# Kernel tuning notes

Measured on AMD Instinct MI355X. Metric: run time of the kernel, lower is better.

## Reference

```python
import jax, jax.numpy as jnp
import numpy as np

D_MODEL = 128
N_HEADS = 8
D_K = D_MODEL // N_HEADS
N_TGT = 40000
N_SRC = 40000
N_EDGES = 640000


def setup_inputs() -> dict:
    key = jax.random.key(0)
    ks = jax.random.split(key, 12)
    s = 1.0 / np.sqrt(D_MODEL)
    return {
        "X_tgt": jax.random.normal(ks[0], (N_TGT, D_MODEL), jnp.float32),
        "X_src": jax.random.normal(ks[1], (N_SRC, D_MODEL), jnp.float32),
        "inc_tgt": jax.random.randint(ks[2], (N_EDGES,), 0, N_TGT),
        "inc_src": jax.random.randint(ks[3], (N_EDGES,), 0, N_SRC),
        "num_tgt": N_TGT,
        # weights stored (in, out): y = x @ W
        "Wq": jax.random.normal(ks[4], (D_MODEL, D_MODEL), jnp.float32) * s,
        "Wkv": jax.random.normal(ks[5], (D_MODEL, 2 * D_MODEL), jnp.float32) * s,
        "Wbt": jax.random.normal(ks[6], (D_MODEL, N_HEADS), jnp.float32) * s,
        "Wbs": jax.random.normal(ks[7], (D_MODEL, N_HEADS), jnp.float32) * s,
        "Wgt_w": jax.random.normal(ks[8], (D_MODEL, D_MODEL), jnp.float32) * s,
        "Wgt_b": jnp.zeros((D_MODEL,), jnp.float32),
        "Wgs_w": jax.random.normal(ks[9], (D_MODEL, D_MODEL), jnp.float32) * s,
        "Wgs_b": jnp.zeros((D_MODEL,), jnp.float32),
        "Wo": jax.random.normal(ks[10], (D_MODEL, D_MODEL), jnp.float32) * s,
    }


def reference(X_tgt, X_src, inc_tgt, inc_src, num_tgt, Wq, Wkv, Wbt, Wbs,
              Wgt_w, Wgt_b, Wgs_w, Wgs_b, Wo):
    H, dk = N_HEADS, D_K
    scale = 1.0 / np.sqrt(dk)
    n_src = X_src.shape[0]

    Q = (X_tgt @ Wq).reshape(-1, H, dk)                 # [Nt,H,dk]
    kv = (X_src @ Wkv).reshape(n_src, 2, H, dk)
    K, V = kv[:, 0], kv[:, 1]                           # [Ns,H,dk]

    # per-edge attention scores [E,H]
    scores = (jnp.sum(Q[inc_tgt] * K[inc_src], axis=-1) * scale
              + (X_tgt @ Wbt)[inc_tgt]
              + (X_src @ Wbs)[inc_src])

    # segment softmax over edges grouped by target node
    mx = jax.ops.segment_max(scores, inc_tgt, num_segments=num_tgt)  # [Nt,H]
    exp_s = jnp.exp(scores - mx[inc_tgt])
    sm = jax.ops.segment_sum(exp_s, inc_tgt, num_segments=num_tgt)
    attn = exp_s / (sm[inc_tgt] + 1e-12)                # [E,H]

    g_src = jax.nn.sigmoid(X_src @ Wgs_w + Wgs_b).reshape(n_src, H, dk)
    msg = attn[..., None] * (g_src[inc_src] * V[inc_src])          # [E,H,dk]
    out = jax.ops.segment_sum(msg, inc_tgt, num_segments=num_tgt)  # [Nt,H,dk]

    g_tgt = jax.nn.sigmoid(X_tgt @ Wgt_w + Wgt_b).reshape(-1, H, dk)
    return (g_tgt * out).reshape(-1, H * dk) @ Wo
```

## Files before the change

### kernel.cpp

```cpp
#include <hip/hip_runtime.h>
#include <math.h>

#define NTGT 40000
#define NSRC 40000
#define NEDGE 640000
#define LOG2E 1.44269504088896f
#define KGROW 256
#define CAP 64

typedef __attribute__((ext_vector_type(8))) short bfrag;
typedef __attribute__((ext_vector_type(4))) short bhalf4;
typedef __attribute__((ext_vector_type(8))) short bhalf8;
typedef __attribute__((ext_vector_type(4))) float f4acc;

__device__ __forceinline__ ushort f2bf(float f) {
  uint u = __float_as_uint(f);
  u += 0x7fffu + ((u >> 16) & 1u);
  return (ushort)(u >> 16);
}
__device__ __forceinline__ float bflo(uint u) { return __uint_as_float(u << 16); }
__device__ __forceinline__ float bfhi(uint u) { return __uint_as_float(u & 0xffff0000u); }
__device__ __forceinline__ float bf2f(short s) { return __uint_as_float(((uint)(ushort)s) << 16); }
__device__ __forceinline__ float sigmoidf_fast(float x) { return 1.0f / (1.0f + __expf(-x)); }

__global__ __launch_bounds__(256) void k_prep(const float* __restrict__ Wq,
                                              const float* __restrict__ Wkv,
                                              const float* __restrict__ Wgt_w,
                                              const float* __restrict__ Wgs_w,
                                              const float* __restrict__ Wo,
                                              const float* __restrict__ Wbs,
                                              int* __restrict__ cntp,
                                              short* __restrict__ WqT, short* __restrict__ WkT,
                                              short* __restrict__ WvT, short* __restrict__ WgtT,
                                              short* __restrict__ WgsT, short* __restrict__ WoT,
                                              short* __restrict__ WbsT) {
  const int b = blockIdx.x;
  const int tid = threadIdx.x;
  if (b >= 7) {
    int i = (b - 7) * 1024 + tid * 4;
    int4 z = {0, 0, 0, 0};
    *reinterpret_cast<int4*>(cntp + i) = z;
    return;
  }
  if (b == 6) {
    for (int idx = tid; idx < 16 * 128; idx += 256) {
      int n = idx >> 7, k = idx & 127;
      WbsT[idx] = (n < 8) ? (short)f2bf(Wbs[k * 8 + n]) : (short)0;
    }
    return;
  }
  __shared__ short T[128][136];
  const float* src;
  int ld, off;
  short* dst;
  switch (b) {
    case 0: src = Wq;    ld = 128; off = 0;   dst = WqT;  break;
    case 1: src = Wkv;   ld = 256; off = 0;   dst = WkT;  break;
    case 2: src = Wkv;   ld = 256; off = 128; dst = WvT;  break;
    case 3: src = Wgt_w; ld = 128; off = 0;   dst = WgtT; break;
    case 4: src = Wgs_w; ld = 128; off = 0;   dst = WgsT; break;
    default:src = Wo;    ld = 128; off = 0;   dst = WoT;  break;
  }
  for (int i = tid; i < 128 * 32; i += 256) {
    int k = i >> 5, c4 = (i & 31) * 4;
    float4 v = *reinterpret_cast<const float4*>(src + (size_t)k * ld + off + c4);
    T[c4 + 0][k] = (short)f2bf(v.x);
    T[c4 + 1][k] = (short)f2bf(v.y);
    T[c4 + 2][k] = (short)f2bf(v.z);
    T[c4 + 3][k] = (short)f2bf(v.w);
  }
  __syncthreads();
  for (int u = tid; u < 128 * 16; u += 256) {
    int n = u >> 4, o = (u & 15) * 8;
    *reinterpret_cast<bhalf8*>(dst + (size_t)n * 128 + o) =
        *reinterpret_cast<const bhalf8*>(&T[n][o]);
  }
}

__global__ __launch_bounds__(512) void k_fill(const int* __restrict__ inc_tgt,
                                              const int* __restrict__ inc_src,
                                              int* __restrict__ cntp,
                                              ushort* __restrict__ elist) {
  const int tid = threadIdx.x;
  const int part = blockIdx.x & 7;
  const int ebase = (blockIdx.x >> 3) * 2000;
#pragma unroll
  for (int k = 0; k < 4; ++k) {
    int off = k * 512 + tid;
    if (off < 2000) {
      int e = ebase + off;
      int t = inc_tgt[e];
      if ((t & 7) == part) {
        int pos = atomicAdd(&cntp[t << 4], 1);
        pos = min(pos, CAP - 1);
        elist[t * CAP + pos] = (ushort)inc_src[e];
      }
    }
  }
}

#define MFMA16(a, b, c) __builtin_amdgcn_mfma_f32_16x16x32_bf16(a, b, c, 0, 0, 0)

__device__ __forceinline__ void stage_issue(const float* __restrict__ X, size_t row0,
                                            float4 ld[4], int tid) {
#pragma unroll
  for (int it = 0; it < 4; ++it) {
    int i = it * 512 + tid;
    int r = i >> 5, c4 = (i & 31) * 4;
    ld[it] = *reinterpret_cast<const float4*>(X + (row0 + r) * 128 + c4);
  }
}
__device__ __forceinline__ void stage_write(short (*Xs)[136], const float4 ld[4], int tid) {
#pragma unroll
  for (int it = 0; it < 4; ++it) {
    int i = it * 512 + tid;
    int r = i >> 5, c4 = (i & 31) * 4;
    bhalf4 o;
    o[0] = (short)f2bf(ld[it].x); o[1] = (short)f2bf(ld[it].y);
    o[2] = (short)f2bf(ld[it].z); o[3] = (short)f2bf(ld[it].w);
    *reinterpret_cast<bhalf4*>(&Xs[r][c4]) = o;
  }
}

__global__ __launch_bounds__(512) void k_proj(const float* __restrict__ Xt,
                                              const float* __restrict__ Xsrc,
                                              const short* __restrict__ WqT,
                                              const short* __restrict__ WgtT,
                                              const short* __restrict__ WkT,
                                              const short* __restrict__ WvT,
                                              const short* __restrict__ WgsT,
                                              const short* __restrict__ WbsT,
                                              const float* __restrict__ Wgt_b,
                                              const float* __restrict__ Wgs_b,
                                              short* __restrict__ Qb, short* __restrict__ gtb,
                                              short* __restrict__ KG,
                                              short* __restrict__ bsb) {
  const int tid = threadIdx.x;
  __shared__ short Xs[2][64][136];
  __shared__ short Stg[2][64][256];
  const int w = tid >> 6, lane = tid & 63;
  const int nl = lane & 15;
  const int kg = (lane >> 4) * 8;
  const int r4 = (lane >> 4) * 4;
  const int c0 = w * 16;
  const bool is_src = blockIdx.x >= 125;
  const int t0 = (is_src ? blockIdx.x - 125 : blockIdx.x) * 5;
  const float* X = is_src ? Xsrc : Xt;

  if (!is_src) {
    bfrag Bq[4], Bg[4];
#pragma unroll
    for (int ks = 0; ks < 4; ++ks) {
      const size_t wo = (size_t)(c0 + nl) * 128 + ks * 32 + kg;
      Bq[ks] = *reinterpret_cast<const bfrag*>(WqT + wo);
      Bg[ks] = *reinterpret_cast<const bfrag*>(WgtT + wo);
    }
    const int c = c0 + nl;
    const float gb = Wgt_b[c];
    {
      float4 ld[4];
      stage_issue(X, (size_t)t0 * 64, ld, tid);
      stage_write(Xs[0], ld, tid);
    }
    __syncthreads();
    int cur = 0;
    for (int ti = 0; ti < 5; ++ti) {
      const size_t row0 = (size_t)(t0 + ti) * 64;
      float4 ld[4];
      if (ti < 4) stage_issue(X, row0 + 64, ld, tid);
      f4acc aQ[4] = {}, aG[4] = {};
#pragma unroll
      for (int ks = 0; ks < 4; ++ks) {
        const int ko = ks * 32 + kg;
        bfrag a0 = *reinterpret_cast<const bfrag*>(&Xs[cur][nl][ko]);
        bfrag a1 = *reinterpret_cast<const bfrag*>(&Xs[cur][16 + nl][ko]);
        bfrag a2 = *reinterpret_cast<const bfrag*>(&Xs[cur][32 + nl][ko]);
        bfrag a3 = *reinterpret_cast<const bfrag*>(&Xs[cur][48 + nl][ko]);
        aQ[0] = MFMA16(a0, Bq[ks], aQ[0]);
        aQ[1] = MFMA16(a1, Bq[ks], aQ[1]);
        aQ[2] = MFMA16(a2, Bq[ks], aQ[2]);
        aQ[3] = MFMA16(a3, Bq[ks], aQ[3]);
        aG[0] = MFMA16(a0, Bg[ks], aG[0]);
        aG[1] = MFMA16(a1, Bg[ks], aG[1]);
        aG[2] = MFMA16(a2, Bg[ks], aG[2]);
        aG[3] = MFMA16(a3, Bg[ks], aG[3]);
      }
#pragma unroll
      for (int rf = 0; rf < 4; ++rf)
#pragma unroll
        for (int j = 0; j < 4; ++j) {
          int r = rf * 16 + r4 + j;
          Stg[cur][r][c] = (short)f2bf(aQ[rf][j] * (0.25f * LOG2E));
          Stg[cur][r][128 + c] = (short)f2bf(sigmoidf_fast(aG[rf][j] + gb));
        }
      if (ti > 0) {
        const size_t rp = (size_t)(t0 + ti - 1) * 64;
        for (int u = tid; u < 1024; u += 512) {
          int r = u >> 4, o = (u & 15) * 8;
          *reinterpret_cast<bhalf8*>(Qb + (rp + r) * 128 + o) =
              *reinterpret_cast<const bhalf8*>(&Stg[cur ^ 1][r][o]);
          *reinterpret_cast<bhalf8*>(gtb + (rp + r) * 128 + o) =
              *reinterpret_cast<const bhalf8*>(&Stg[cur ^ 1][r][128 + o]);
        }
      }
      if (ti < 4) stage_write(Xs[cur ^ 1], ld, tid);
      __syncthreads();
      cur ^= 1;
    }
    {
      const size_t rp = (size_t)(t0 + 4) * 64;
      for (int u = tid; u < 1024; u += 512) {
        int r = u >> 4, o = (u & 15) * 8;
        *reinterpret_cast<bhalf8*>(Qb + (rp + r) * 128 + o) =
            *reinterpret_cast<const bhalf8*>(&Stg[cur ^ 1][r][o]);
        *reinterpret_cast<bhalf8*>(gtb + (rp + r) * 128 + o) =
            *reinterpret_cast<const bhalf8*>(&Stg[cur ^ 1][r][128 + o]);
      }
    }
  } else {
    bfrag Bk[4], Bv[4], Bg[4], Bb[4];
#pragma unroll
    for (int ks = 0; ks < 4; ++ks) {
      const size_t wo = (size_t)(c0 + nl) * 128 + ks * 32 + kg;
      Bk[ks] = *reinterpret_cast<const bfrag*>(WkT + wo);
      Bv[ks] = *reinterpret_cast<const bfrag*>(WvT + wo);
      Bg[ks] = *reinterpret_cast<const bfrag*>(WgsT + wo);
      Bb[ks] = *reinterpret_cast<const bfrag*>(WbsT + (size_t)nl * 128 + ks * 32 + kg);
    }
    const int c = c0 + nl;
    const int slot = (c >> 1) * 4 + (c & 1);
    const float gb = Wgs_b[c];
    {
      float4 ld[4];
      stage_issue(X, (size_t)t0 * 64, ld, tid);
      stage_write(Xs[0], ld, tid);
    }
    __syncthreads();
    int cur = 0;
    for (int ti = 0; ti < 5; ++ti) {
      const size_t row0 = (size_t)(t0 + ti) * 64;
      float4 ld[4];
      if (ti < 4) stage_issue(X, row0 + 64, ld, tid);
      f4acc aK[4] = {}, aV[4] = {}, aG[4] = {}, aB[4] = {};
#pragma unroll
      for (int ks = 0; ks < 4; ++ks) {
        const int ko = ks * 32 + kg;
        bfrag a0 = *reinterpret_cast<const bfrag*>(&Xs[cur][nl][ko]);
        bfrag a1 = *reinterpret_cast<const bfrag*>(&Xs[cur][16 + nl][ko]);
        bfrag a2 = *reinterpret_cast<const bfrag*>(&Xs[cur][32 + nl][ko]);
        bfrag a3 = *reinterpret_cast<const bfrag*>(&Xs[cur][48 + nl][ko]);
        aK[0] = MFMA16(a0, Bk[ks], aK[0]);
        aK[1] = MFMA16(a1, Bk[ks], aK[1]);
        aK[2] = MFMA16(a2, Bk[ks], aK[2]);
        aK[3] = MFMA16(a3, Bk[ks], aK[3]);
        aV[0] = MFMA16(a0, Bv[ks], aV[0]);
        aV[1] = MFMA16(a1, Bv[ks], aV[1]);
        aV[2] = MFMA16(a2, Bv[ks], aV[2]);
        aV[3] = MFMA16(a3, Bv[ks], aV[3]);
        aG[0] = MFMA16(a0, Bg[ks], aG[0]);
        aG[1] = MFMA16(a1, Bg[ks], aG[1]);
        aG[2] = MFMA16(a2, Bg[ks], aG[2]);
        aG[3] = MFMA16(a3, Bg[ks], aG[3]);
        if (w == 0) {
          aB[0] = MFMA16(a0, Bb[ks], aB[0]);
          aB[1] = MFMA16(a1, Bb[ks], aB[1]);
          aB[2] = MFMA16(a2, Bb[ks], aB[2]);
          aB[3] = MFMA16(a3, Bb[ks], aB[3]);
        }
      }
#pragma unroll
      for (int rf = 0; rf < 4; ++rf)
#pragma unroll
        for (int j = 0; j < 4; ++j) {
          int r = rf * 16 + r4 + j;
          float g = sigmoidf_fast(aG[rf][j] + gb);
          Stg[cur][r][slot] = (short)f2bf(aK[rf][j]);
          Stg[cur][r][slot + 2] = (short)f2bf(g * aV[rf][j]);
        }
      if (w == 0 && nl < 8) {
#pragma unroll
        for (int rf = 0; rf < 4; ++rf)
#pragma unroll
          for (int j = 0; j < 4; ++j)
            bsb[(row0 + rf * 16 + r4 + j) * 8 + nl] = (short)f2bf(aB[rf][j] * LOG2E);
      }
      if (ti > 0) {
        const size_t rp = (size_t)(t0 + ti - 1) * 64;
        for (int u = tid; u < 2048; u += 512) {
          int r = u >> 5, o = (u & 31) * 8;
          *reinterpret_cast<bhalf8*>(KG + (rp + r) * KGROW + o) =
              *reinterpret_cast<const bhalf8*>(&Stg[cur ^ 1][r][o]);
        }
      }
      if (ti < 4) stage_write(Xs[cur ^ 1], ld, tid);
      __syncthreads();
      cur ^= 1;
    }
    {
      const size_t rp = (size_t)(t0 + 4) * 64;
      for (int u = tid; u < 2048; u += 512) {
        int r = u >> 5, o = (u & 31) * 8;
        *reinterpret_cast<bhalf8*>(KG + (rp + r) * KGROW + o) =
            *reinterpret_cast<const bhalf8*>(&Stg[cur ^ 1][r][o]);
      }
    }
  }
}

__global__ __launch_bounds__(256) void k_attn(const uint2* __restrict__ Qp2,
                                              const uint4* __restrict__ KGp4,
                                              const short* __restrict__ bsb,
                                              const uint2* __restrict__ gtp2,
                                              const int* __restrict__ cntp,
                                              const ushort* __restrict__ elist,
                                              uint2* __restrict__ tmpp2) {
  const int wave = threadIdx.x >> 6;
  const int lane = threadIdx.x & 63;
  const int t = blockIdx.x * 4 + wave;
  const int p = lane & 31;
  const int h = p >> 2;
  const int hi = lane >> 5;

  uint2 qv = Qp2[(size_t)t * 32 + p];
  float q0 = bflo(qv.x), q1 = bfhi(qv.x), q2 = bflo(qv.y), q3 = bfhi(qv.y);
  const int deg = min(cntp[t << 4], CAP);
  const int ebase = t * CAP;

  float ssum = 0.f, a0 = 0.f, a1 = 0.f, a2 = 0.f, a3 = 0.f;
  int i = 0;
  for (; i + 8 <= deg; i += 8) {
    int sv[4];
    uint4 kv[4];
    float bv[4], dd[4];
#pragma unroll
    for (int u = 0; u < 4; ++u) sv[u] = (int)elist[ebase + i + 2 * u + hi];
#pragma unroll
    for (int u = 0; u < 4; ++u) {
      kv[u] = KGp4[(size_t)sv[u] * 32 + p];
      bv[u] = bf2f(bsb[(size_t)sv[u] * 8 + h]);
    }
#pragma unroll
    for (int u = 0; u < 4; ++u)
      dd[u] = q0 * bflo(kv[u].x) + q1 * bfhi(kv[u].x) + q2 * bflo(kv[u].z) + q3 * bfhi(kv[u].z);
#pragma unroll
    for (int u = 0; u < 4; ++u) dd[u] += __shfl_xor(dd[u], 1);
#pragma unroll
    for (int u = 0; u < 4; ++u) dd[u] += __shfl_xor(dd[u], 2);
#pragma unroll
    for (int u = 0; u < 4; ++u) {
      float e = __builtin_amdgcn_exp2f(dd[u] + bv[u]);
      ssum += e;
      a0 = fmaf(e, bflo(kv[u].y), a0);
      a1 = fmaf(e, bfhi(kv[u].y), a1);
      a2 = fmaf(e, bflo(kv[u].w), a2);
      a3 = fmaf(e, bfhi(kv[u].w), a3);
    }
  }
  for (; i < deg; i += 2) {
    int idx = i + hi;
    float pen = 0.f;
    if (idx >= deg) { idx = deg - 1; pen = -1e30f; }
    int s = (int)elist[ebase + idx];
    uint4 kv = KGp4[(size_t)s * 32 + p];
    float bsv = bf2f(bsb[(size_t)s * 8 + h]);
    float d = q0 * bflo(kv.x) + q1 * bfhi(kv.x) + q2 * bflo(kv.z) + q3 * bfhi(kv.z);
    d += __shfl_xor(d, 1);
    d += __shfl_xor(d, 2);
    float e = __builtin_amdgcn_exp2f(d + bsv + pen);
    ssum += e;
    a0 = fmaf(e, bflo(kv.y), a0);
    a1 = fmaf(e, bfhi(kv.y), a1);
    a2 = fmaf(e, bflo(kv.w), a2);
    a3 = fmaf(e, bfhi(kv.w), a3);
  }
  ssum += __shfl_xor(ssum, 32);
  a0 += __shfl_xor(a0, 32);
  a1 += __shfl_xor(a1, 32);
  a2 += __shfl_xor(a2, 32);
  a3 += __shfl_xor(a3, 32);
  if (lane < 32) {
    float inv = 1.f / (ssum + 1e-12f);
    uint2 g2 = gtp2[(size_t)t * 32 + p];
    float o0 = bflo(g2.x) * a0 * inv;
    float o1 = bfhi(g2.x) * a1 * inv;
    float o2 = bflo(g2.y) * a2 * inv;
    float o3 = bfhi(g2.y) * a3 * inv;
    uint2 pk;
    pk.x = ((uint)f2bf(o0)) | (((uint)f2bf(o1)) << 16);
    pk.y = ((uint)f2bf(o2)) | (((uint)f2bf(o3)) << 16);
    tmpp2[(size_t)t * 32 + p] = pk;
  }
}

__device__ __forceinline__ void stage_rows_bf16(const short* __restrict__ X, size_t row0,
                                                short (*Xs)[136], int tid) {
  for (int i = tid; i < 64 * 32; i += 256) {
    int r = i >> 5, c4 = (i & 31) * 4;
    *reinterpret_cast<bhalf4*>(&Xs[r][c4]) =
        *reinterpret_cast<const bhalf4*>(X + (row0 + r) * 128 + c4);
  }
}

__device__ __forceinline__ void mfma_pass(const short (*Xs)[136], int wave, int lane,
                                          const short* __restrict__ WT, f4acc acc[8]) {
  const int rl = wave * 16 + (lane & 15);
  const int kg = (lane >> 4) * 8;
  const int nl = lane & 15;
#pragma unroll
  for (int ks = 0; ks < 4; ++ks) {
    bfrag a = *reinterpret_cast<const bfrag*>(&Xs[rl][ks * 32 + kg]);
#pragma unroll
    for (int nf = 0; nf < 8; ++nf) {
      bfrag b = *reinterpret_cast<const bfrag*>(WT + (size_t)(nf * 16 + nl) * 128 + ks * 32 + kg);
      acc[nf] = MFMA16(a, b, acc[nf]);
    }
  }
}

__global__ __launch_bounds__(256) void k_out(const short* __restrict__ tmpb,
                                             const short* __restrict__ WoT,
                                             float* __restrict__ out) {
  __shared__ short Xs[64][136];
  const int tid = threadIdx.x;
  const size_t row0 = (size_t)blockIdx.x * 64;
  stage_rows_bf16(tmpb, row0, Xs, tid);
  __syncthreads();
  const int wave = tid >> 6, lane = tid & 63;
  const int rbase = (int)row0 + wave * 16 + ((lane >> 4) << 2);
  const int cl = lane & 15;
  f4acc acc[8] = {};
  mfma_pass(Xs, wave, lane, WoT, acc);
#pragma unroll
  for (int nf = 0; nf < 8; ++nf)
#pragma unroll
    for (int j = 0; j < 4; ++j)
      out[(size_t)(rbase + j) * 128 + nf * 16 + cl] = acc[nf][j];
}

extern "C" void kernel_launch(void* const* d_in, const int* in_sizes, int n_in,
                              void* d_out, int out_size, void* d_ws, size_t ws_size,
                              hipStream_t stream) {
  const float* X_tgt = (const float*)d_in[0];
  const float* X_src = (const float*)d_in[1];
  const int* inc_tgt = (const int*)d_in[2];
  const int* inc_src = (const int*)d_in[3];
  const float* Wq    = (const float*)d_in[5];
  const float* Wkv   = (const float*)d_in[6];
  const float* Wbs   = (const float*)d_in[8];
  const float* Wgt_w = (const float*)d_in[9];
  const float* Wgt_b = (const float*)d_in[10];
  const float* Wgs_w = (const float*)d_in[11];
  const float* Wgs_b = (const float*)d_in[12];
  const float* Wo    = (const float*)d_in[13];
  float* out = (float*)d_out;

  char* ws = (char*)d_ws;
  short* Qb   = (short*)ws; ws += (size_t)NTGT * 128 * 2;
  short* KG   = (short*)ws; ws += (size_t)NSRC * KGROW * 2;
  short* gtb  = (short*)ws; ws += (size_t)NTGT * 128 * 2;
  short* tmpb = (short*)ws; ws += (size_t)NTGT * 128 * 2;
  short* bsb  = (short*)ws; ws += (size_t)NSRC * 8 * 2;
  int* cntp  = (int*)ws; ws += (size_t)NTGT * 16 * 4;
  ushort* elist = (ushort*)ws; ws += (size_t)NTGT * CAP * 2;
  short* WqT  = (short*)ws; ws += 128 * 128 * 2;
  short* WkT  = (short*)ws; ws += 128 * 128 * 2;
  short* WvT  = (short*)ws; ws += 128 * 128 * 2;
  short* WgtT = (short*)ws; ws += 128 * 128 * 2;
  short* WgsT = (short*)ws; ws += 128 * 128 * 2;
  short* WoT  = (short*)ws; ws += 128 * 128 * 2;
  short* WbsT = (short*)ws; ws += 16 * 128 * 2;

  k_prep<<<632, 256, 0, stream>>>(Wq, Wkv, Wgt_w, Wgs_w, Wo, Wbs, cntp,
                                  WqT, WkT, WvT, WgtT, WgsT, WoT, WbsT);
  k_fill<<<2560, 512, 0, stream>>>(inc_tgt, inc_src, cntp, elist);
  k_proj<<<250, 512, 0, stream>>>(X_tgt, X_src, WqT, WgtT, WkT, WvT, WgsT,
                                  WbsT, Wgt_b, Wgs_b, Qb, gtb, KG, bsb);
  k_attn<<<NTGT / 4, 256, 0, stream>>>((const uint2*)Qb, (const uint4*)KG, bsb,
                                       (const uint2*)gtb, cntp, elist, (uint2*)tmpb);
  k_out<<<NTGT / 64, 256, 0, stream>>>(tmpb, WoT, out);
}
```

Measured before the change: 128.4 us.

## Fuse attention aggregation with output projection via shared-memory tile

Merges k_attn and k_out into one kernel: each 512-thread block handles 64 targets, with 8 waves each processing 8 targets sequentially and writing the gated result into a shared tile. After a barrier, 4 waves run the MFMA projection with Wo directly to the output. This removes the intermediate bf16 buffer round-trip through global memory and one kernel launch. In exchange, only 625 blocks exist, each wave processes 8 targets serially, and half the waves sit idle during the matmul phase, which may reduce latency hiding for the gather-bound attention loop.

Measured after the change: 124.8 us. 2.8% less time.

```diff
diff --git a/kernel.cpp b/kernel.cpp
--- a/kernel.cpp
+++ b/kernel.cpp
@@ -307,134 +307,121 @@
   }
 }
 
-__global__ __launch_bounds__(256) void k_attn(const uint2* __restrict__ Qp2,
+__device__ __forceinline__ void mfma_pass(const short (*Xs)[136], int wave, int lane,
+                                          const short* __restrict__ WT, f4acc acc[8]) {
+  const int rl = wave * 16 + (lane & 15);
+  const int kg = (lane >> 4) * 8;
+  const int nl = lane & 15;
+#pragma unroll
+  for (int ks = 0; ks < 4; ++ks) {
+    bfrag a = *reinterpret_cast<const bfrag*>(&Xs[rl][ks * 32 + kg]);
+#pragma unroll
+    for (int nf = 0; nf < 8; ++nf) {
+      bfrag b = *reinterpret_cast<const bfrag*>(WT + (size_t)(nf * 16 + nl) * 128 + ks * 32 + kg);
+      acc[nf] = MFMA16(a, b, acc[nf]);
+    }
+  }
+}
+
+__global__ __launch_bounds__(512) void k_attn(const uint2* __restrict__ Qp2,
                                               const uint4* __restrict__ KGp4,
                                               const short* __restrict__ bsb,
                                               const uint2* __restrict__ gtp2,
                                               const int* __restrict__ cntp,
                                               const ushort* __restrict__ elist,
-                                              uint2* __restrict__ tmpp2) {
-  const int wave = threadIdx.x >> 6;
-  const int lane = threadIdx.x & 63;
-  const int t = blockIdx.x * 4 + wave;
+                                              const short* __restrict__ WoT,
+                                              float* __restrict__ out) {
+  __shared__ short T[64][136];
+  const int tid = threadIdx.x;
+  const int w = tid >> 6;
+  const int lane = tid & 63;
   const int p = lane & 31;
   const int h = p >> 2;
   const int hi = lane >> 5;
-
-  uint2 qv = Qp2[(size_t)t * 32 + p];
-  float q0 = bflo(qv.x), q1 = bfhi(qv.x), q2 = bflo(qv.y), q3 = bfhi(qv.y);
-  const int deg = min(cntp[t << 4], CAP);
-  const int ebase = t * CAP;
-
-  float ssum = 0.f, a0 = 0.f, a1 = 0.f, a2 = 0.f, a3 = 0.f;
-  int i = 0;
-  for (; i + 8 <= deg; i += 8) {
-    int sv[4];
-    uint4 kv[4];
-    float bv[4], dd[4];
-#pragma unroll
-    for (int u = 0; u < 4; ++u) sv[u] = (int)elist[ebase + i + 2 * u + hi];
-#pragma unroll
-    for (int u = 0; u < 4; ++u) {
-      kv[u] = KGp4[(size_t)sv[u] * 32 + p];
-      bv[u] = bf2f(bsb[(size_t)sv[u] * 8 + h]);
-    }
-#pragma unroll
-    for (int u = 0; u < 4; ++u)
-      dd[u] = q0 * bflo(kv[u].x) + q1 * bfhi(kv[u].x) + q2 * bflo(kv[u].z) + q3 * bfhi(kv[u].z);
-#pragma unroll
-    for (int u = 0; u < 4; ++u) dd[u] += __shfl_xor(dd[u], 1);
-#pragma unroll
-    for (int u = 0; u < 4; ++u) dd[u] += __shfl_xor(dd[u], 2);
-#pragma unroll
-    for (int u = 0; u < 4; ++u) {
-      float e = __builtin_amdgcn_exp2f(dd[u] + bv[u]);
+  const int tb = blockIdx.x * 64;
+
+  for (int tt = 0; tt < 8; ++tt) {
+    const int t = tb + w * 8 + tt;
+    uint2 qv = Qp2[(size_t)t * 32 + p];
+    float q0 = bflo(qv.x), q1 = bfhi(qv.x), q2 = bflo(qv.y), q3 = bfhi(qv.y);
+    const int deg = min(cntp[t << 4], CAP);
+    const int ebase = t * CAP;
+
+    float ssum = 0.f, a0 = 0.f, a1 = 0.f, a2 = 0.f, a3 = 0.f;
+    int i = 0;
+    for (; i + 8 <= deg; i += 8) {
+      int sv[4];
+      uint4 kv[4];
+      float bv[4], dd[4];
+#pragma unroll
+      for (int u = 0; u < 4; ++u) sv[u] = (int)elist[ebase + i + 2 * u + hi];
+#pragma unroll
+      for (int u = 0; u < 4; ++u) {
+        kv[u] = KGp4[(size_t)sv[u] * 32 + p];
+        bv[u] = bf2f(bsb[(size_t)sv[u] * 8 + h]);
+      }
+#pragma unroll
+      for (int u = 0; u < 4; ++u)
+        dd[u] = q0 * bflo(kv[u].x) + q1 * bfhi(kv[u].x) + q2 * bflo(kv[u].z) + q3 * bfhi(kv[u].z);
+#pragma unroll
+      for (int u = 0; u < 4; ++u) dd[u] += __shfl_xor(dd[u], 1);
+#pragma unroll
+      for (int u = 0; u < 4; ++u) dd[u] += __shfl_xor(dd[u], 2);
+#pragma unroll
+      for (int u = 0; u < 4; ++u) {
+        float e = __builtin_amdgcn_exp2f(dd[u] + bv[u]);
+        ssum += e;
+        a0 = fmaf(e, bflo(kv[u].y), a0);
+        a1 = fmaf(e, bfhi(kv[u].y), a1);
+        a2 = fmaf(e, bflo(kv[u].w), a2);
+        a3 = fmaf(e, bfhi(kv[u].w), a3);
+      }
+    }
+    for (; i < deg; i += 2) {
+      int idx = i + hi;
+      float pen = 0.f;
+      if (idx >= deg) { idx = deg - 1; pen = -1e30f; }
+      int s = (int)elist[ebase + idx];
+      uint4 kv = KGp4[(size_t)s * 32 + p];
+      float bsv = bf2f(bsb[(size_t)s * 8 + h]);
+      float d = q0 * bflo(kv.x) + q1 * bfhi(kv.x) + q2 * bflo(kv.z) + q3 * bfhi(kv.z);
+      d += __shfl_xor(d, 1);
+      d += __shfl_xor(d, 2);
+      float e = __builtin_amdgcn_exp2f(d + bsv + pen);
       ssum += e;
-      a0 = fmaf(e, bflo(kv[u].y), a0);
-      a1 = fmaf(e, bfhi(kv[u].y), a1);
-      a2 = fmaf(e, bflo(kv[u].w), a2);
-      a3 = fmaf(e, bfhi(kv[u].w), a3);
-    }
-  }
-  for (; i < deg; i += 2) {
-    int idx = i + hi;
-    float pen = 0.f;
-    if (idx >= deg) { idx = deg - 1; pen = -1e30f; }
-    int s = (int)elist[ebase + idx];
-    uint4 kv = KGp4[(size_t)s * 32 + p];
-    float bsv = bf2f(bsb[(size_t)s * 8 + h]);
-    float d = q0 * bflo(kv.x) + q1 * bfhi(kv.x) + q2 * bflo(kv.z) + q3 * bfhi(kv.z);
-    d += __shfl_xor(d, 1);
-    d += __shfl_xor(d, 2);
-    float e = __builtin_amdgcn_exp2f(d + bsv + pen);
-    ssum += e;
-    a0 = fmaf(e, bflo(kv.y), a0);
-    a1 = fmaf(e, bfhi(kv.y), a1);
-    a2 = fmaf(e, bflo(kv.w), a2);
-    a3 = fmaf(e, bfhi(kv.w), a3);
-  }
-  ssum += __shfl_xor(ssum, 32);
-  a0 += __shfl_xor(a0, 32);
-  a1 += __shfl_xor(a1, 32);
-  a2 += __shfl_xor(a2, 32);
-  a3 += __shfl_xor(a3, 32);
-  if (lane < 32) {
-    float inv = 1.f / (ssum + 1e-12f);
-    uint2 g2 = gtp2[(size_t)t * 32 + p];
-    float o0 = bflo(g2.x) * a0 * inv;
-    float o1 = bfhi(g2.x) * a1 * inv;
-    float o2 = bflo(g2.y) * a2 * inv;
-    float o3 = bfhi(g2.y) * a3 * inv;
-    uint2 pk;
-    pk.x = ((uint)f2bf(o0)) | (((uint)f2bf(o1)) << 16);
-    pk.y = ((uint)f2bf(o2)) | (((uint)f2bf(o3)) << 16);
-    tmpp2[(size_t)t * 32 + p] = pk;
-  }
-}
-
-__device__ __forceinline__ void stage_rows_bf16(const short* __restrict__ X, size_t row0,
-                                                short (*Xs)[136], int tid) {
-  for (int i = tid; i < 64 * 32; i += 256) {
-    int r = i >> 5, c4 = (i & 31) * 4;
-    *reinterpret_cast<bhalf4*>(&Xs[r][c4]) =
-        *reinterpret_cast<const bhalf4*>(X + (row0 + r) * 128 + c4);
-  }
-}
-
-__device__ __forceinline__ void mfma_pass(const short (*Xs)[136], int wave, int lane,
-                                          const short* __restrict__ WT, f4acc acc[8]) {
-  const int rl = wave * 16 + (lane & 15);
-  const int kg = (lane >> 4) * 8;
-  const int nl = lane & 15;
-#pragma unroll
-  for (int ks = 0; ks < 4; ++ks) {
-    bfrag a = *reinterpret_cast<const bfrag*>(&Xs[rl][ks * 32 + kg]);
-#pragma unroll
-    for (int nf = 0; nf < 8; ++nf) {
-      bfrag b = *reinterpret_cast<const bfrag*>(WT + (size_t)(nf * 16 + nl) * 128 + ks * 32 + kg);
-      acc[nf] = MFMA16(a, b, acc[nf]);
-    }
-  }
-}
-
-__global__ __launch_bounds__(256) void k_out(const short* __restrict__ tmpb,
-                                             const short* __restrict__ WoT,
-                                             float* __restrict__ out) {
-  __shared__ short Xs[64][136];
-  const int tid = threadIdx.x;
-  const size_t row0 = (size_t)blockIdx.x * 64;
-  stage_rows_bf16(tmpb, row0, Xs, tid);
+      a0 = fmaf(e, bflo(kv.y), a0);
+      a1 = fmaf(e, bfhi(kv.y), a1);
+      a2 = fmaf(e, bflo(kv.w), a2);
+      a3 = fmaf(e, bfhi(kv.w), a3);
+    }
+    ssum += __shfl_xor(ssum, 32);
+    a0 += __shfl_xor(a0, 32);
+    a1 += __shfl_xor(a1, 32);
+    a2 += __shfl_xor(a2, 32);
+    a3 += __shfl_xor(a3, 32);
+    if (lane < 32) {
+      float inv = 1.f / (ssum + 1e-12f);
+      uint2 g2 = gtp2[(size_t)t * 32 + p];
+      bhalf4 pk;
+      pk[0] = (short)f2bf(bflo(g2.x) * a0 * inv);
+      pk[1] = (short)f2bf(bfhi(g2.x) * a1 * inv);
+      pk[2] = (short)f2bf(bflo(g2.y) * a2 * inv);
+      pk[3] = (short)f2bf(bfhi(g2.y) * a3 * inv);
+      *reinterpret_cast<bhalf4*>(&T[w * 8 + tt][p * 4]) = pk;
+    }
+  }
   __syncthreads();
-  const int wave = tid >> 6, lane = tid & 63;
-  const int rbase = (int)row0 + wave * 16 + ((lane >> 4) << 2);
-  const int cl = lane & 15;
-  f4acc acc[8] = {};
-  mfma_pass(Xs, wave, lane, WoT, acc);
-#pragma unroll
-  for (int nf = 0; nf < 8; ++nf)
-#pragma unroll
-    for (int j = 0; j < 4; ++j)
-      out[(size_t)(rbase + j) * 128 + nf * 16 + cl] = acc[nf][j];
+  if (w < 4) {
+    f4acc acc[8] = {};
+    mfma_pass(T, w, lane, WoT, acc);
+    const int rbase = tb + w * 16 + ((lane >> 4) << 2);
+    const int cl = lane & 15;
+#pragma unroll
+    for (int nf = 0; nf < 8; ++nf)
+#pragma unroll
+      for (int j = 0; j < 4; ++j)
+        out[(size_t)(rbase + j) * 128 + nf * 16 + cl] = acc[nf][j];
+  }
 }
 
 extern "C" void kernel_launch(void* const* d_in, const int* in_sizes, int n_in,
@@ -458,7 +445,6 @@
   short* Qb   = (short*)ws; ws += (size_t)NTGT * 128 * 2;
   short* KG   = (short*)ws; ws += (size_t)NSRC * KGROW * 2;
   short* gtb  = (short*)ws; ws += (size_t)NTGT * 128 * 2;
-  short* tmpb = (short*)ws; ws += (size_t)NTGT * 128 * 2;
   short* bsb  = (short*)ws; ws += (size_t)NSRC * 8 * 2;
   int* cntp  = (int*)ws; ws += (size_t)NTGT * 16 * 4;
   ushort* elist = (ushort*)ws; ws += (size_t)NTGT * CAP * 2;
@@ -475,7 +461,6 @@
   k_fill<<<2560, 512, 0, stream>>>(inc_tgt, inc_src, cntp, elist);
   k_proj<<<250, 512, 0, stream>>>(X_tgt, X_src, WqT, WgtT, WkT, WvT, WgsT,
                                   WbsT, Wgt_b, Wgs_b, Qb, gtb, KG, bsb);
-  k_attn<<<NTGT / 4, 256, 0, stream>>>((const uint2*)Qb, (const uint4*)KG, bsb,
-                                       (const uint2*)gtb, cntp, elist, (uint2*)tmpb);
-  k_out<<<NTGT / 64, 256, 0, stream>>>(tmpb, WoT, out);
-}
+  k_attn<<<NTGT / 64, 512, 0, stream>>>((const uint2*)Qb, (const uint4*)KG, bsb,
+                                        (const uint2*)gtb, cntp, elist, WoT, out);
+}
```
